# Optimization experiments

Hardware: AMD Instinct MI355X
Metric: run time of the kernel (lower is better)

The kernel has to match this reference:

```python
import jax, jax.numpy as jnp
import numpy as np

N_NODES = 50000
N_EDGES = 800000
N_FIELDS = 4
N_MESH = 8
HIDDEN = 128
IN_CH = N_FIELDS * 1 + N_MESH  # 12


def _w(key, shape, scale=0.05):
    return jax.random.normal(key, shape, dtype=jnp.float32) * scale


def setup_inputs() -> dict:
    key = jax.random.key(0)
    ks = jax.random.split(key, 20)
    inp = {
        "F_0": jax.random.normal(ks[0], (N_NODES, 1, N_FIELDS), dtype=jnp.float32),
        "meshfield": jax.random.normal(ks[1], (N_NODES, N_MESH), dtype=jnp.float32),
        "edge_index": jax.random.randint(ks[2], (2, N_EDGES), 0, N_NODES, dtype=jnp.int32),
        "n_timesteps": 8,
        # encoder SAGEConv 1: in 12 -> 128 ; SAGEConv 2: 128 -> 128
        "enc1_Wl": _w(ks[3], (HIDDEN, IN_CH)), "enc1_bl": jnp.zeros((HIDDEN,), jnp.float32), "enc1_Wr": _w(ks[4], (HIDDEN, IN_CH)),
        "enc2_Wl": _w(ks[5], (HIDDEN, HIDDEN)), "enc2_bl": jnp.zeros((HIDDEN,), jnp.float32), "enc2_Wr": _w(ks[6], (HIDDEN, HIDDEN)),
        # decoder SAGEConv 1 & 2: 128 -> 128
        "dec1_Wl": _w(ks[7], (HIDDEN, HIDDEN)), "dec1_bl": jnp.zeros((HIDDEN,), jnp.float32), "dec1_Wr": _w(ks[8], (HIDDEN, HIDDEN)),
        "dec2_Wl": _w(ks[9], (HIDDEN, HIDDEN)), "dec2_bl": jnp.zeros((HIDDEN,), jnp.float32), "dec2_Wr": _w(ks[10], (HIDDEN, HIDDEN)),
        # output head: 128 -> n_fields
        "lin_W": _w(ks[11], (N_FIELDS, HIDDEN)), "lin_b": jnp.zeros((N_FIELDS,), jnp.float32),
    }
    return inp


def sage_conv(x, src, dst, Wl, bl, Wr, n_nodes):
    # PyG SAGEConv: out = lin_l(mean_j x_j) + lin_r(x_i); lin_l has bias, lin_r does not.
    msg = x[src]                                             # [E, C] gather
    agg = jax.ops.segment_sum(msg, dst, num_segments=n_nodes)
    cnt = jax.ops.segment_sum(jnp.ones((src.shape[0], 1), x.dtype), dst, num_segments=n_nodes)
    agg = agg / jnp.maximum(cnt, 1.0)                        # scatter-mean
    return agg @ Wl.T + bl + x @ Wr.T


def reference(F_0, meshfield, edge_index, n_timesteps,
              enc1_Wl, enc1_bl, enc1_Wr, enc2_Wl, enc2_bl, enc2_Wr,
              dec1_Wl, dec1_bl, dec1_Wr, dec2_Wl, dec2_bl, dec2_Wr,
              lin_W, lin_b):
    n = F_0.shape[0]
    src, dst = edge_index[0], edge_index[1]
    relu = jax.nn.relu
    F_prev = F_0  # [N, n_prev=1, n_fields]
    outs = []
    for _ in range(int(n_timesteps)):
        x_prev = F_prev[:, -1]                               # [N, n_fields]
        x = jnp.concatenate([F_prev.reshape(n, -1), meshfield], axis=1)  # [N, 12]
        # encoder GraphSAGE (act between layers, none after last)
        h = relu(sage_conv(x, src, dst, enc1_Wl, enc1_bl, enc1_Wr, n))
        h = sage_conv(h, src, dst, enc2_Wl, enc2_bl, enc2_Wr, n)
        h = relu(h)                                          # self.act after encoder
        # decoder GraphSAGE
        h = relu(sage_conv(h, src, dst, dec1_Wl, dec1_bl, dec1_Wr, n))
        h = sage_conv(h, src, dst, dec2_Wl, dec2_bl, dec2_Wr, n)
        h = relu(h)                                          # self.act after decoder
        x_new = x_prev + h @ lin_W.T + lin_b                 # residual update
        outs.append(x_new[:, None, :])
        # recurrence uses detached prediction (x.detach() in torch)
        F_prev = jnp.concatenate([F_prev[:, 1:], jax.lax.stop_gradient(x_new)[:, None, :]], axis=1)
    return jnp.concatenate(outs, axis=1)                     # [N, n_timesteps, n_fields]
```

## Files before the change

### kernel.cpp

```cpp
#include <hip/hip_runtime.h>


typedef __attribute__((ext_vector_type(8))) short short8;
typedef __attribute__((ext_vector_type(8))) unsigned short ushort8;
typedef __attribute__((ext_vector_type(4))) float f32x4;

static __device__ __forceinline__ float b2f(unsigned short u) {
  return __uint_as_float(((unsigned int)u) << 16);
}
static __device__ __forceinline__ unsigned short f2bf(float f) {
  unsigned int u = __float_as_uint(f);
  u += 0x7FFFu + ((u >> 16) & 1u);
  return (unsigned short)(u >> 16);
}


__global__ void count_deg_kernel(const int* __restrict__ dst, int* __restrict__ cnt, int E) {
  int e = blockIdx.x * blockDim.x + threadIdx.x;
  if (e < E) atomicAdd(&cnt[dst[e]], 1);
}

__global__ __launch_bounds__(256) void blocksum_kernel(const int* __restrict__ cnt,
                                                       int* __restrict__ bsum, int n) {
  __shared__ int s[256];
  int tid = threadIdx.x;
  int i = blockIdx.x * 256 + tid;
  s[tid] = (i < n) ? cnt[i] : 0;
  __syncthreads();
  for (int off = 128; off > 0; off >>= 1) {
    if (tid < off) s[tid] += s[tid + off];
    __syncthreads();
  }
  if (tid == 0) bsum[blockIdx.x] = s[0];
}

__global__ __launch_bounds__(256) void scan_sums_kernel(const int* __restrict__ bsum,
                                                        int* __restrict__ boff, int nb) {
  __shared__ int s[256];
  int tid = threadIdx.x;
  int v = (tid < nb) ? bsum[tid] : 0;
  s[tid] = v;
  __syncthreads();
  for (int off = 1; off < 256; off <<= 1) {
    int t = (tid >= off) ? s[tid - off] : 0;
    __syncthreads();
    s[tid] += t;
    __syncthreads();
  }
  if (tid < nb) boff[tid] = s[tid] - v;
}

__global__ __launch_bounds__(256) void expand_kernel(const int* __restrict__ cnt,
                                                     const int* __restrict__ boff,
                                                     int* __restrict__ row_ptr,
                                                     float* __restrict__ rdeg, int n) {
  __shared__ int s[256];
  int tid = threadIdx.x;
  int i = blockIdx.x * 256 + tid;
  int v = (i < n) ? cnt[i] : 0;
  s[tid] = v;
  __syncthreads();
  for (int off = 1; off < 256; off <<= 1) {
    int t = (tid >= off) ? s[tid - off] : 0;
    __syncthreads();
    s[tid] += t;
    __syncthreads();
  }
  if (i < n) {
    row_ptr[i + 1] = boff[blockIdx.x] + s[tid];
    rdeg[i] = 1.0f / fmaxf((float)v, 1.0f);
  }
  if (i == 0) row_ptr[0] = 0;
}

__global__ void fill_csr_kernel(const int* __restrict__ src, const int* __restrict__ dst,
                                const int* __restrict__ row_ptr, int* __restrict__ cursor,
                                int* __restrict__ col, int E) {
  int e = blockIdx.x * blockDim.x + threadIdx.x;
  if (e < E) {
    int d = dst[e];
    int p = atomicAdd(&cursor[d], 1);
    col[row_ptr[d] + p] = src[e];
  }
}

__global__ void f2bf6_kernel(const float* __restrict__ s0, const float* __restrict__ s1,
                             const float* __restrict__ s2, const float* __restrict__ s3,
                             const float* __restrict__ s4, const float* __restrict__ s5,
                             unsigned short* __restrict__ dst) {
  int i = blockIdx.x * blockDim.x + threadIdx.x;
  if (i >= 6 * 16384) return;
  int m = i >> 14, o = i & 16383;
  const float* s;
  switch (m) {
    case 0: s = s0; break; case 1: s = s1; break; case 2: s = s2; break;
    case 3: s = s3; break; case 4: s = s4; break; default: s = s5; break;
  }
  dst[i] = f2bf(s[o]);
}


__global__ __launch_bounds__(256) void enc1_kernel(
    const float* __restrict__ xprev, const float* __restrict__ mesh,
    const int* __restrict__ row_ptr, const int* __restrict__ col,
    const float* __restrict__ rdeg,
    const float* __restrict__ Wl, const float* __restrict__ Wr,
    const float* __restrict__ bl, unsigned short* __restrict__ out, int N) {
  __shared__ float Ws[24][128];
  __shared__ float As[16][24];
  int tid = threadIdx.x;
  int nb = blockIdx.x * 16;
  for (int i = tid; i < 1536; i += 256) {
    int o = i / 12, k = i % 12;
    Ws[k][o] = Wl[i];
    Ws[12 + k][o] = Wr[i];
  }
  if (tid < 192) {
    int n = tid / 12, k = tid % 12;
    int gn = nb + n; if (gn > N - 1) gn = N - 1;
    float own = (k < 4) ? xprev[gn * 4 + k] : mesh[gn * 8 + (k - 4)];
    As[n][12 + k] = own;
    int j0 = row_ptr[gn], j1 = row_ptr[gn + 1];
    float acc = 0.0f;
    int j = j0;
    for (; j + 2 <= j1; j += 2) {
      int s0 = col[j], s1 = col[j + 1];
      float v0 = (k < 4) ? xprev[s0 * 4 + k] : mesh[s0 * 8 + (k - 4)];
      float v1 = (k < 4) ? xprev[s1 * 4 + k] : mesh[s1 * 8 + (k - 4)];
      acc += v0 + v1;
    }
    if (j < j1) {
      int s0 = col[j];
      acc += (k < 4) ? xprev[s0 * 4 + k] : mesh[s0 * 8 + (k - 4)];
    }
    As[n][k] = acc * rdeg[gn];
  }
  __syncthreads();
  int nl = tid >> 4;
  int og = tid & 15;
  float acc[8] = {};
#pragma unroll
  for (int k = 0; k < 24; ++k) {
    float a = As[nl][k];
    float4 w0 = *(const float4*)&Ws[k][og * 8];
    float4 w1 = *(const float4*)&Ws[k][og * 8 + 4];
    acc[0] += a * w0.x; acc[1] += a * w0.y; acc[2] += a * w0.z; acc[3] += a * w0.w;
    acc[4] += a * w1.x; acc[5] += a * w1.y; acc[6] += a * w1.z; acc[7] += a * w1.w;
  }
  int gn = nb + nl;
  if (gn < N) {
#pragma unroll
    for (int j = 0; j < 8; ++j) {
      float v = acc[j] + bl[og * 8 + j];
      out[gn * 128 + og * 8 + j] = f2bf(fmaxf(v, 0.0f));
    }
  }
}

__global__ void agg128_kernel(const unsigned short* __restrict__ feat,
                              unsigned short* __restrict__ out,
                              const int* __restrict__ row_ptr, const int* __restrict__ col,
                              const float* __restrict__ rdeg, int N) {
  int g = blockIdx.x * blockDim.x + threadIdx.x;
  int node = g >> 4;
  int d = g & 15;
  if (node >= N) return;
  int j0 = row_ptr[node], j1 = row_ptr[node + 1];
  float acc[8] = {};
  int j = j0;
  for (; j + 4 <= j1; j += 4) {
    int s0 = col[j], s1 = col[j + 1], s2 = col[j + 2], s3 = col[j + 3];
    ushort8 v0 = *(const ushort8*)&feat[s0 * 128 + d * 8];
    ushort8 v1 = *(const ushort8*)&feat[s1 * 128 + d * 8];
    ushort8 v2 = *(const ushort8*)&feat[s2 * 128 + d * 8];
    ushort8 v3 = *(const ushort8*)&feat[s3 * 128 + d * 8];
#pragma unroll
    for (int r = 0; r < 8; ++r)
      acc[r] += (b2f(v0[r]) + b2f(v1[r])) + (b2f(v2[r]) + b2f(v3[r]));
  }
  for (; j < j1; ++j) {
    ushort8 v0 = *(const ushort8*)&feat[col[j] * 128 + d * 8];
#pragma unroll
    for (int r = 0; r < 8; ++r) acc[r] += b2f(v0[r]);
  }
  float rd = rdeg[node];
  ushort8 o;
#pragma unroll
  for (int r = 0; r < 8; ++r) o[r] = f2bf(acc[r] * rd);
  *(ushort8*)&out[node * 128 + d * 8] = o;
}

__global__ __launch_bounds__(256) void gemm128_mfma_kernel(
    const unsigned short* __restrict__ agg, const unsigned short* __restrict__ x,
    const unsigned short* __restrict__ Wlb, const unsigned short* __restrict__ Wrb,
    const float* __restrict__ bl, unsigned short* __restrict__ out, int N) {
  int tid = threadIdx.x;
  int wave = tid >> 6;
  int lane = tid & 63;
  int nb = blockIdx.x * 128 + wave * 32;
  int l15 = lane & 15;
  int lk = (lane >> 4) * 8;

  f32x4 acc[2][8] = {};
  int r0 = nb + l15;      if (r0 > N - 1) r0 = N - 1;
  int r1 = nb + 16 + l15; if (r1 > N - 1) r1 = N - 1;

#pragma unroll
  for (int ks = 0; ks < 8; ++ks) {
    const unsigned short* As = (ks < 4) ? agg : x;
    const unsigned short* Ws = (ks < 4) ? Wlb : Wrb;
    int ko = (ks & 3) * 32 + lk;
    short8 a0 = *(const short8*)&As[r0 * 128 + ko];
    short8 a1 = *(const short8*)&As[r1 * 128 + ko];
#pragma unroll
    for (int ot = 0; ot < 8; ++ot) {
      short8 b = *(const short8*)&Ws[(ot * 16 + l15) * 128 + ko];
      acc[0][ot] = __builtin_amdgcn_mfma_f32_16x16x32_bf16(a0, b, acc[0][ot], 0, 0, 0);
      acc[1][ot] = __builtin_amdgcn_mfma_f32_16x16x32_bf16(a1, b, acc[1][ot], 0, 0, 0);
    }
  }

  int crow = (lane >> 4) * 4;
#pragma unroll
  for (int ot = 0; ot < 8; ++ot) {
    int gcol = ot * 16 + l15;
    float bv = bl[gcol];
#pragma unroll
    for (int mt = 0; mt < 2; ++mt) {
#pragma unroll
      for (int r = 0; r < 4; ++r) {
        int grow = nb + mt * 16 + crow + r;
        if (grow < N) {
          float v = fmaxf(acc[mt][ot][r] + bv, 0.0f);
          out[grow * 128 + gcol] = f2bf(v);
        }
      }
    }
  }
}

__global__ __launch_bounds__(256) void gemm128_head_mfma_kernel(
    const unsigned short* __restrict__ agg, const unsigned short* __restrict__ x,
    const unsigned short* __restrict__ Wlb, const unsigned short* __restrict__ Wrb,
    const float* __restrict__ bl, const float* __restrict__ linW,
    const float* __restrict__ linb, float* __restrict__ xprev,
    float* __restrict__ out, int N, int T, int t) {
  __shared__ float Wh[4][128];
  int tid = threadIdx.x;
  for (int i = tid; i < 512; i += 256) Wh[i >> 7][i & 127] = linW[i];
  __syncthreads();

  int wave = tid >> 6;
  int lane = tid & 63;
  int nb = blockIdx.x * 128 + wave * 32;
  int l15 = lane & 15;
  int lk = (lane >> 4) * 8;

  f32x4 acc[2][8] = {};
  int r0 = nb + l15;      if (r0 > N - 1) r0 = N - 1;
  int r1 = nb + 16 + l15; if (r1 > N - 1) r1 = N - 1;

#pragma unroll
  for (int ks = 0; ks < 8; ++ks) {
    const unsigned short* As = (ks < 4) ? agg : x;
    const unsigned short* Ws = (ks < 4) ? Wlb : Wrb;
    int ko = (ks & 3) * 32 + lk;
    short8 a0 = *(const short8*)&As[r0 * 128 + ko];
    short8 a1 = *(const short8*)&As[r1 * 128 + ko];
#pragma unroll
    for (int ot = 0; ot < 8; ++ot) {
      short8 b = *(const short8*)&Ws[(ot * 16 + l15) * 128 + ko];
      acc[0][ot] = __builtin_amdgcn_mfma_f32_16x16x32_bf16(a0, b, acc[0][ot], 0, 0, 0);
      acc[1][ot] = __builtin_amdgcn_mfma_f32_16x16x32_bf16(a1, b, acc[1][ot], 0, 0, 0);
    }
  }

  float part[2][4][4] = {};
#pragma unroll
  for (int ot = 0; ot < 8; ++ot) {
    int gcol = ot * 16 + l15;
    float bv = bl[gcol];
    float w0 = Wh[0][gcol], w1 = Wh[1][gcol], w2 = Wh[2][gcol], w3 = Wh[3][gcol];
#pragma unroll
    for (int mt = 0; mt < 2; ++mt)
#pragma unroll
      for (int r = 0; r < 4; ++r) {
        float hv = fmaxf(acc[mt][ot][r] + bv, 0.0f);
        part[mt][r][0] += hv * w0;
        part[mt][r][1] += hv * w1;
        part[mt][r][2] += hv * w2;
        part[mt][r][3] += hv * w3;
      }
  }
#pragma unroll
  for (int m = 1; m < 16; m <<= 1)
#pragma unroll
    for (int mt = 0; mt < 2; ++mt)
#pragma unroll
      for (int r = 0; r < 4; ++r)
#pragma unroll
        for (int o = 0; o < 4; ++o)
          part[mt][r][o] += __shfl_xor(part[mt][r][o], m, 64);

  if (l15 == 0) {
    int crow = (lane >> 4) * 4;
    float4 lb = *(const float4*)linb;
#pragma unroll
    for (int mt = 0; mt < 2; ++mt)
#pragma unroll
      for (int r = 0; r < 4; ++r) {
        int grow = nb + mt * 16 + crow + r;
        if (grow < N) {
          float4 xp = *(const float4*)&xprev[grow * 4];
          float4 xn;
          xn.x = xp.x + part[mt][r][0] + lb.x;
          xn.y = xp.y + part[mt][r][1] + lb.y;
          xn.z = xp.z + part[mt][r][2] + lb.z;
          xn.w = xp.w + part[mt][r][3] + lb.w;
          *(float4*)&out[(grow * T + t) * 4] = xn;
          *(float4*)&xprev[grow * 4] = xn;
        }
      }
  }
}

extern "C" void kernel_launch(void* const* d_in, const int* in_sizes, int n_in,
                              void* d_out, int out_size, void* d_ws, size_t ws_size,
                              hipStream_t stream) {
  const float* F0   = (const float*)d_in[0];
  const float* mesh = (const float*)d_in[1];
  const int*   eidx = (const int*)d_in[2];
  const float* e1Wl = (const float*)d_in[4];
  const float* e1bl = (const float*)d_in[5];
  const float* e1Wr = (const float*)d_in[6];
  const float* e2Wl = (const float*)d_in[7];
  const float* e2bl = (const float*)d_in[8];
  const float* e2Wr = (const float*)d_in[9];
  const float* d1Wl = (const float*)d_in[10];
  const float* d1bl = (const float*)d_in[11];
  const float* d1Wr = (const float*)d_in[12];
  const float* d2Wl = (const float*)d_in[13];
  const float* d2bl = (const float*)d_in[14];
  const float* d2Wr = (const float*)d_in[15];
  const float* linW = (const float*)d_in[16];
  const float* linb = (const float*)d_in[17];

  const int N = in_sizes[0] / 4;
  const int E = in_sizes[2] / 2;
  const int T = out_size / (N * 4);
  const int* src = eidx;
  const int* dst = eidx + E;

  size_t off = 0;
  auto alloc = [&](size_t bytes) -> void* {
    void* p = (char*)d_ws + off;
    off += (bytes + 511) & ~(size_t)511;
    return p;
  };
  int*   cnt     = (int*)alloc((size_t)N * 4);
  int*   row_ptr = (int*)alloc((size_t)(N + 1) * 4);
  int*   cursor  = (int*)alloc((size_t)N * 4);
  int*   col     = (int*)alloc((size_t)E * 4);
  float* rdeg    = (float*)alloc((size_t)N * 4);
  float* xprev   = (float*)alloc((size_t)N * 4 * 4);
  int*   bsum    = (int*)alloc(256 * 4);
  int*   boff    = (int*)alloc(256 * 4);
  unsigned short* h1   = (unsigned short*)alloc((size_t)N * 128 * 2);
  unsigned short* h2   = (unsigned short*)alloc((size_t)N * 128 * 2);
  unsigned short* aggb = (unsigned short*)alloc((size_t)N * 128 * 2);
  unsigned short* wb   = (unsigned short*)alloc((size_t)6 * 128 * 128 * 2);
  unsigned short* e2Wlb = wb + 0 * 16384;
  unsigned short* e2Wrb = wb + 1 * 16384;
  unsigned short* d1Wlb = wb + 2 * 16384;
  unsigned short* d1Wrb = wb + 3 * 16384;
  unsigned short* d2Wlb = wb + 4 * 16384;
  unsigned short* d2Wrb = wb + 5 * 16384;

  float* outp = (float*)d_out;

  const int NB = (N + 255) / 256;

  hipMemsetAsync(cnt, 0, (size_t)N * 4, stream);
  hipMemsetAsync(cursor, 0, (size_t)N * 4, stream);
  count_deg_kernel<<<(E + 255) / 256, 256, 0, stream>>>(dst, cnt, E);
  blocksum_kernel<<<NB, 256, 0, stream>>>(cnt, bsum, N);
  scan_sums_kernel<<<1, 256, 0, stream>>>(bsum, boff, NB);
  expand_kernel<<<NB, 256, 0, stream>>>(cnt, boff, row_ptr, rdeg, N);
  fill_csr_kernel<<<(E + 255) / 256, 256, 0, stream>>>(src, dst, row_ptr, cursor, col, E);
  f2bf6_kernel<<<(6 * 16384 + 255) / 256, 256, 0, stream>>>(
      e2Wl, e2Wr, d1Wl, d1Wr, d2Wl, d2Wr, wb);
  hipMemcpyAsync(xprev, F0, (size_t)N * 4 * 4, hipMemcpyDeviceToDevice, stream);

  const int gAgg  = (N * 16 + 255) / 256;
  const int gGemm = (N + 127) / 128;
  const int gEnc1 = (N + 15) / 16;

  for (int t = 0; t < T; ++t) {
    enc1_kernel<<<gEnc1, 256, 0, stream>>>(xprev, mesh, row_ptr, col, rdeg,
                                           e1Wl, e1Wr, e1bl, h1, N);

    agg128_kernel<<<gAgg, 256, 0, stream>>>(h1, aggb, row_ptr, col, rdeg, N);
    gemm128_mfma_kernel<<<gGemm, 256, 0, stream>>>(aggb, h1, e2Wlb, e2Wrb, e2bl, h2, N);

    agg128_kernel<<<gAgg, 256, 0, stream>>>(h2, aggb, row_ptr, col, rdeg, N);
    gemm128_mfma_kernel<<<gGemm, 256, 0, stream>>>(aggb, h2, d1Wlb, d1Wrb, d1bl, h1, N);

    agg128_kernel<<<gAgg, 256, 0, stream>>>(h1, aggb, row_ptr, col, rdeg, N);
    gemm128_head_mfma_kernel<<<gGemm, 256, 0, stream>>>(aggb, h1, d2Wlb, d2Wrb, d2bl,
                                                        linW, linb, xprev, outp, N, T, t);
  }
}
```

Baseline: 1.735 ms.

## Precompute time-invariant mesh term for enc1, fuse CSR rank, unroll aggregation

The meshfield contribution to the first encoder layer (its aggregation, its linear terms and the bias) does not change across timesteps. It is now computed once into a bf16 buffer before the loop, so each per-timestep enc1 pass only gathers the 4-wide previous state and adds the cached term. CSR construction records each edge's rank during degree counting, which removes the second atomic pass and the cursor buffer. The 128-wide aggregation gather is unrolled to 8 neighbours to keep more loads in flight. The cached mesh term is stored as bf16, which adds rounding compared with the previous fp32 path, and it costs an extra N×128 buffer.

```diff
diff --git a/kernel.cpp b/kernel.cpp
--- a/kernel.cpp
+++ b/kernel.cpp
@@ -15,9 +15,10 @@
 }
 
 
-__global__ void count_deg_kernel(const int* __restrict__ dst, int* __restrict__ cnt, int E) {
+__global__ void count_rank_kernel(const int* __restrict__ dst, int* __restrict__ cnt,
+                                  int* __restrict__ rank, int E) {
   int e = blockIdx.x * blockDim.x + threadIdx.x;
-  if (e < E) atomicAdd(&cnt[dst[e]], 1);
+  if (e < E) rank[e] = atomicAdd(&cnt[dst[e]], 1);
 }
 
 __global__ __launch_bounds__(256) void blocksum_kernel(const int* __restrict__ cnt,
@@ -73,15 +74,11 @@
   if (i == 0) row_ptr[0] = 0;
 }
 
-__global__ void fill_csr_kernel(const int* __restrict__ src, const int* __restrict__ dst,
-                                const int* __restrict__ row_ptr, int* __restrict__ cursor,
-                                int* __restrict__ col, int E) {
+__global__ void fill_csr2_kernel(const int* __restrict__ src, const int* __restrict__ dst,
+                                 const int* __restrict__ rank, const int* __restrict__ row_ptr,
+                                 int* __restrict__ col, int E) {
   int e = blockIdx.x * blockDim.x + threadIdx.x;
-  if (e < E) {
-    int d = dst[e];
-    int p = atomicAdd(&cursor[d], 1);
-    col[row_ptr[d] + p] = src[e];
-  }
+  if (e < E) col[row_ptr[dst[e]] + rank[e]] = src[e];
 }
 
 __global__ void f2bf6_kernel(const float* __restrict__ s0, const float* __restrict__ s1,
@@ -99,61 +96,115 @@
   dst[i] = f2bf(s[o]);
 }
 
+__global__ void aggmesh_kernel(const float* __restrict__ mesh, float* __restrict__ aggm,
+                               const int* __restrict__ row_ptr, const int* __restrict__ col,
+                               const float* __restrict__ rdeg, int N) {
+  int g = blockIdx.x * blockDim.x + threadIdx.x;
+  int node = g >> 1, h = (g & 1) * 4;
+  if (node >= N) return;
+  int j0 = row_ptr[node], j1 = row_ptr[node + 1];
+  float4 acc = make_float4(0.f, 0.f, 0.f, 0.f);
+  int j = j0;
+  for (; j + 4 <= j1; j += 4) {
+    float4 v0 = *(const float4*)&mesh[col[j] * 8 + h];
+    float4 v1 = *(const float4*)&mesh[col[j + 1] * 8 + h];
+    float4 v2 = *(const float4*)&mesh[col[j + 2] * 8 + h];
+    float4 v3 = *(const float4*)&mesh[col[j + 3] * 8 + h];
+    acc.x += (v0.x + v1.x) + (v2.x + v3.x);
+    acc.y += (v0.y + v1.y) + (v2.y + v3.y);
+    acc.z += (v0.z + v1.z) + (v2.z + v3.z);
+    acc.w += (v0.w + v1.w) + (v2.w + v3.w);
+  }
+  for (; j < j1; ++j) {
+    float4 v0 = *(const float4*)&mesh[col[j] * 8 + h];
+    acc.x += v0.x; acc.y += v0.y; acc.z += v0.z; acc.w += v0.w;
+  }
+  float r = rdeg[node];
+  acc.x *= r; acc.y *= r; acc.z *= r; acc.w *= r;
+  *(float4*)&aggm[node * 8 + h] = acc;
+}
+
+__global__ void mesh_term_kernel(const float* __restrict__ aggm, const float* __restrict__ mesh,
+                                 const float* __restrict__ Wl, const float* __restrict__ Wr,
+                                 const float* __restrict__ bl, unsigned short* __restrict__ mterm,
+                                 int N) {
+  int g = blockIdx.x * blockDim.x + threadIdx.x;
+  if (g >= N * 128) return;
+  int n = g >> 7, o = g & 127;
+  float acc = bl[o];
+#pragma unroll
+  for (int k = 0; k < 8; ++k)
+    acc += Wl[o * 12 + 4 + k] * aggm[n * 8 + k] + Wr[o * 12 + 4 + k] * mesh[n * 8 + k];
+  mterm[g] = f2bf(acc);
+}
+
 
 __global__ __launch_bounds__(256) void enc1_kernel(
-    const float* __restrict__ xprev, const float* __restrict__ mesh,
-    const int* __restrict__ row_ptr, const int* __restrict__ col,
-    const float* __restrict__ rdeg,
+    const float* __restrict__ xprev, const int* __restrict__ row_ptr,
+    const int* __restrict__ col, const float* __restrict__ rdeg,
     const float* __restrict__ Wl, const float* __restrict__ Wr,
-    const float* __restrict__ bl, unsigned short* __restrict__ out, int N) {
-  __shared__ float Ws[24][128];
-  __shared__ float As[16][24];
-  int tid = threadIdx.x;
-  int nb = blockIdx.x * 16;
-  for (int i = tid; i < 1536; i += 256) {
-    int o = i / 12, k = i % 12;
-    Ws[k][o] = Wl[i];
-    Ws[12 + k][o] = Wr[i];
-  }
-  if (tid < 192) {
-    int n = tid / 12, k = tid % 12;
-    int gn = nb + n; if (gn > N - 1) gn = N - 1;
-    float own = (k < 4) ? xprev[gn * 4 + k] : mesh[gn * 8 + (k - 4)];
-    As[n][12 + k] = own;
-    int j0 = row_ptr[gn], j1 = row_ptr[gn + 1];
-    float acc = 0.0f;
-    int j = j0;
-    for (; j + 2 <= j1; j += 2) {
-      int s0 = col[j], s1 = col[j + 1];
-      float v0 = (k < 4) ? xprev[s0 * 4 + k] : mesh[s0 * 8 + (k - 4)];
-      float v1 = (k < 4) ? xprev[s1 * 4 + k] : mesh[s1 * 8 + (k - 4)];
-      acc += v0 + v1;
+    const unsigned short* __restrict__ mterm, unsigned short* __restrict__ out, int N) {
+  __shared__ float Wx[8][128];
+  __shared__ float4 part[256];
+  __shared__ float As[64][8];
+  int tid = threadIdx.x;
+  int nb = blockIdx.x * 64;
+  for (int i = tid; i < 1024; i += 256) {
+    int k = i >> 7, o = i & 127;
+    Wx[k][o] = (k < 4) ? Wl[o * 12 + k] : Wr[o * 12 + (k - 4)];
+  }
+  int nl = tid >> 2, q = tid & 3;
+  int gn = nb + nl; if (gn > N - 1) gn = N - 1;
+  int j0 = row_ptr[gn], j1 = row_ptr[gn + 1];
+  int per = (j1 - j0 + 3) >> 2;
+  int a = j0 + q * per; if (a > j1) a = j1;
+  int b = a + per; if (b > j1) b = j1;
+  float4 acc = make_float4(0.f, 0.f, 0.f, 0.f);
+  int j = a;
+  for (; j + 2 <= b; j += 2) {
+    float4 v0 = *(const float4*)&xprev[col[j] * 4];
+    float4 v1 = *(const float4*)&xprev[col[j + 1] * 4];
+    acc.x += v0.x + v1.x; acc.y += v0.y + v1.y;
+    acc.z += v0.z + v1.z; acc.w += v0.w + v1.w;
+  }
+  if (j < b) {
+    float4 v0 = *(const float4*)&xprev[col[j] * 4];
+    acc.x += v0.x; acc.y += v0.y; acc.z += v0.z; acc.w += v0.w;
+  }
+  part[tid] = acc;
+  __syncthreads();
+  if (tid < 64) {
+    int g2 = nb + tid; if (g2 > N - 1) g2 = N - 1;
+    float4 s0 = part[tid * 4], s1 = part[tid * 4 + 1];
+    float4 s2 = part[tid * 4 + 2], s3 = part[tid * 4 + 3];
+    float r = rdeg[g2];
+    As[tid][0] = (s0.x + s1.x + s2.x + s3.x) * r;
+    As[tid][1] = (s0.y + s1.y + s2.y + s3.y) * r;
+    As[tid][2] = (s0.z + s1.z + s2.z + s3.z) * r;
+    As[tid][3] = (s0.w + s1.w + s2.w + s3.w) * r;
+    float4 own = *(const float4*)&xprev[g2 * 4];
+    As[tid][4] = own.x; As[tid][5] = own.y; As[tid][6] = own.z; As[tid][7] = own.w;
+  }
+  __syncthreads();
+  int gn2 = nb + nl;
+  if (gn2 >= N) return;
+  float av[8];
+#pragma unroll
+  for (int k = 0; k < 8; ++k) av[k] = As[nl][k];
+  int o0 = q * 32;
+#pragma unroll
+  for (int c = 0; c < 4; ++c) {
+    ushort8 mt = *(const ushort8*)&mterm[gn2 * 128 + o0 + c * 8];
+    ushort8 ov;
+#pragma unroll
+    for (int oo = 0; oo < 8; ++oo) {
+      int o = o0 + c * 8 + oo;
+      float s = b2f(mt[oo]);
+#pragma unroll
+      for (int k = 0; k < 8; ++k) s += av[k] * Wx[k][o];
+      ov[oo] = f2bf(fmaxf(s, 0.0f));
     }
-    if (j < j1) {
-      int s0 = col[j];
-      acc += (k < 4) ? xprev[s0 * 4 + k] : mesh[s0 * 8 + (k - 4)];
-    }
-    As[n][k] = acc * rdeg[gn];
-  }
-  __syncthreads();
-  int nl = tid >> 4;
-  int og = tid & 15;
-  float acc[8] = {};
-#pragma unroll
-  for (int k = 0; k < 24; ++k) {
-    float a = As[nl][k];
-    float4 w0 = *(const float4*)&Ws[k][og * 8];
-    float4 w1 = *(const float4*)&Ws[k][og * 8 + 4];
-    acc[0] += a * w0.x; acc[1] += a * w0.y; acc[2] += a * w0.z; acc[3] += a * w0.w;
-    acc[4] += a * w1.x; acc[5] += a * w1.y; acc[6] += a * w1.z; acc[7] += a * w1.w;
-  }
-  int gn = nb + nl;
-  if (gn < N) {
-#pragma unroll
-    for (int j = 0; j < 8; ++j) {
-      float v = acc[j] + bl[og * 8 + j];
-      out[gn * 128 + og * 8 + j] = f2bf(fmaxf(v, 0.0f));
-    }
+    *(ushort8*)&out[gn2 * 128 + o0 + c * 8] = ov;
   }
 }
 
@@ -168,17 +219,27 @@
   int j0 = row_ptr[node], j1 = row_ptr[node + 1];
   float acc[8] = {};
   int j = j0;
-  for (; j + 4 <= j1; j += 4) {
-    int s0 = col[j], s1 = col[j + 1], s2 = col[j + 2], s3 = col[j + 3];
-    ushort8 v0 = *(const ushort8*)&feat[s0 * 128 + d * 8];
-    ushort8 v1 = *(const ushort8*)&feat[s1 * 128 + d * 8];
-    ushort8 v2 = *(const ushort8*)&feat[s2 * 128 + d * 8];
-    ushort8 v3 = *(const ushort8*)&feat[s3 * 128 + d * 8];
+  for (; j + 8 <= j1; j += 8) {
+    ushort8 v0 = *(const ushort8*)&feat[col[j    ] * 128 + d * 8];
+    ushort8 v1 = *(const ushort8*)&feat[col[j + 1] * 128 + d * 8];
+    ushort8 v2 = *(const ushort8*)&feat[col[j + 2] * 128 + d * 8];
+    ushort8 v3 = *(const ushort8*)&feat[col[j + 3] * 128 + d * 8];
+    ushort8 v4 = *(const ushort8*)&feat[col[j + 4] * 128 + d * 8];
+    ushort8 v5 = *(const ushort8*)&feat[col[j + 5] * 128 + d * 8];
+    ushort8 v6 = *(const ushort8*)&feat[col[j + 6] * 128 + d * 8];
+    ushort8 v7 = *(const ushort8*)&feat[col[j + 7] * 128 + d * 8];
 #pragma unroll
     for (int r = 0; r < 8; ++r)
-      acc[r] += (b2f(v0[r]) + b2f(v1[r])) + (b2f(v2[r]) + b2f(v3[r]));
-  }
-  for (; j < j1; ++j) {
+      acc[r] += ((b2f(v0[r]) + b2f(v1[r])) + (b2f(v2[r]) + b2f(v3[r]))) +
+                ((b2f(v4[r]) + b2f(v5[r])) + (b2f(v6[r]) + b2f(v7[r])));
+  }
+  for (; j + 2 <= j1; j += 2) {
+    ushort8 v0 = *(const ushort8*)&feat[col[j] * 128 + d * 8];
+    ushort8 v1 = *(const ushort8*)&feat[col[j + 1] * 128 + d * 8];
+#pragma unroll
+    for (int r = 0; r < 8; ++r) acc[r] += b2f(v0[r]) + b2f(v1[r]);
+  }
+  if (j < j1) {
     ushort8 v0 = *(const ushort8*)&feat[col[j] * 128 + d * 8];
 #pragma unroll
     for (int r = 0; r < 8; ++r) acc[r] += b2f(v0[r]);
@@ -359,12 +420,14 @@
   };
   int*   cnt     = (int*)alloc((size_t)N * 4);
   int*   row_ptr = (int*)alloc((size_t)(N + 1) * 4);
-  int*   cursor  = (int*)alloc((size_t)N * 4);
+  int*   rank    = (int*)alloc((size_t)E * 4);
   int*   col     = (int*)alloc((size_t)E * 4);
   float* rdeg    = (float*)alloc((size_t)N * 4);
   float* xprev   = (float*)alloc((size_t)N * 4 * 4);
+  float* aggm    = (float*)alloc((size_t)N * 8 * 4);
   int*   bsum    = (int*)alloc(256 * 4);
   int*   boff    = (int*)alloc(256 * 4);
+  unsigned short* mterm = (unsigned short*)alloc((size_t)N * 128 * 2);
   unsigned short* h1   = (unsigned short*)alloc((size_t)N * 128 * 2);
   unsigned short* h2   = (unsigned short*)alloc((size_t)N * 128 * 2);
   unsigned short* aggb = (unsigned short*)alloc((size_t)N * 128 * 2);
@@ -381,23 +444,25 @@
   const int NB = (N + 255) / 256;
 
   hipMemsetAsync(cnt, 0, (size_t)N * 4, stream);
-  hipMemsetAsync(cursor, 0, (size_t)N * 4, stream);
-  count_deg_kernel<<<(E + 255) / 256, 256, 0, stream>>>(dst, cnt, E);
+  count_rank_kernel<<<(E + 255) / 256, 256, 0, stream>>>(dst, cnt, rank, E);
   blocksum_kernel<<<NB, 256, 0, stream>>>(cnt, bsum, N);
   scan_sums_kernel<<<1, 256, 0, stream>>>(bsum, boff, NB);
   expand_kernel<<<NB, 256, 0, stream>>>(cnt, boff, row_ptr, rdeg, N);
-  fill_csr_kernel<<<(E + 255) / 256, 256, 0, stream>>>(src, dst, row_ptr, cursor, col, E);
+  fill_csr2_kernel<<<(E + 255) / 256, 256, 0, stream>>>(src, dst, rank, row_ptr, col, E);
   f2bf6_kernel<<<(6 * 16384 + 255) / 256, 256, 0, stream>>>(
       e2Wl, e2Wr, d1Wl, d1Wr, d2Wl, d2Wr, wb);
+  aggmesh_kernel<<<(N * 2 + 255) / 256, 256, 0, stream>>>(mesh, aggm, row_ptr, col, rdeg, N);
+  mesh_term_kernel<<<(N * 128 + 255) / 256, 256, 0, stream>>>(aggm, mesh, e1Wl, e1Wr, e1bl,
+                                                              mterm, N);
   hipMemcpyAsync(xprev, F0, (size_t)N * 4 * 4, hipMemcpyDeviceToDevice, stream);
 
   const int gAgg  = (N * 16 + 255) / 256;
   const int gGemm = (N + 127) / 128;
-  const int gEnc1 = (N + 15) / 16;
+  const int gEnc1 = (N + 63) / 64;
 
   for (int t = 0; t < T; ++t) {
-    enc1_kernel<<<gEnc1, 256, 0, stream>>>(xprev, mesh, row_ptr, col, rdeg,
-                                           e1Wl, e1Wr, e1bl, h1, N);
+    enc1_kernel<<<gEnc1, 256, 0, stream>>>(xprev, row_ptr, col, rdeg,
+                                           e1Wl, e1Wr, mterm, h1, N);
 
     agg128_kernel<<<gAgg, 256, 0, stream>>>(h1, aggb, row_ptr, col, rdeg, N);
     gemm128_mfma_kernel<<<gGemm, 256, 0, stream>>>(aggb, h1, e2Wlb, e2Wrb, e2bl, h2, N);
```

Result: faster. 1.642 ms, median of 2 (-5.4%).
